# Optimization experiments

Hardware: AMD Instinct MI355X
Metric: run time of the kernel (lower is better)

## Reference

```python
import jax, jax.numpy as jnp
import numpy as np

N_NODES = 50000
N_EDGES = 400000
N_GRAPHS = 128
IN_DIM = 768
HID = 128
N_CLASSES = 11
BN_EPS = 1e-5


def _sage_conv(x, src, dst, Wl, bl, Wr):
    # PyG SAGEConv (aggr='mean'): out = lin_l(mean_{j->i} x_j) + lin_r(x_i)
    # messages flow src -> dst; nodes with no in-edges get a zero aggregate.
    n = x.shape[0]
    deg = jax.ops.segment_sum(jnp.ones_like(dst, x.dtype), dst, num_segments=n)
    agg = jax.ops.segment_sum(x[src], dst, num_segments=n)  # [N, d] gather+scatter
    agg = agg / jnp.maximum(deg, 1.0)[:, None]
    return agg @ Wl.T + bl + x @ Wr.T


def _batch_norm(x, gamma, beta):
    # training-mode BatchNorm1d: biased batch statistics over the node axis
    m = jnp.mean(x, axis=0)
    v = jnp.var(x, axis=0)
    return (x - m) * jax.lax.rsqrt(v + BN_EPS) * gamma + beta


def setup_inputs() -> dict:
    key = jax.random.key(0)
    ks = jax.random.split(key, 16)
    x = jax.random.normal(ks[0], (N_NODES, IN_DIM), dtype=jnp.float32)
    edge_index = jax.random.randint(ks[1], (2, N_EDGES), 0, N_NODES, dtype=jnp.int32)
    batch = jnp.sort(jax.random.randint(ks[2], (N_NODES,), 0, N_GRAPHS, dtype=jnp.int32))

    def lin_w(k, out_d, in_d):
        return jax.random.normal(k, (out_d, in_d), dtype=jnp.float32) * (1.0 / np.sqrt(in_d))

    params = {
        'W1l': lin_w(ks[3], HID, IN_DIM), 'b1': jnp.zeros((HID,), jnp.float32),
        'W1r': lin_w(ks[4], HID, IN_DIM),
        'g1': jnp.ones((HID,), jnp.float32), 'be1': jnp.zeros((HID,), jnp.float32),
        'W2l': lin_w(ks[5], HID, HID), 'b2': jnp.zeros((HID,), jnp.float32),
        'W2r': lin_w(ks[6], HID, HID),
        'g2': jnp.ones((HID,), jnp.float32), 'be2': jnp.zeros((HID,), jnp.float32),
        'W3l': lin_w(ks[7], HID, HID), 'b3': jnp.zeros((HID,), jnp.float32),
        'W3r': lin_w(ks[8], HID, HID),
        'g3': jnp.ones((HID,), jnp.float32), 'be3': jnp.zeros((HID,), jnp.float32),
        'Wlin': lin_w(ks[9], N_CLASSES, HID), 'blin': jnp.zeros((N_CLASSES,), jnp.float32),
    }
    return {'x': x, 'edge_index': edge_index, 'batch': batch, **params}


def reference(x, edge_index, batch,
              W1l, b1, W1r, g1, be1,
              W2l, b2, W2r, g2, be2,
              W3l, b3, W3r, g3, be3,
              Wlin, blin):
    src, dst = edge_index[0], edge_index[1]
    h = jax.nn.relu(_batch_norm(_sage_conv(x, src, dst, W1l, b1, W1r), g1, be1))
    h = jax.nn.relu(_batch_norm(_sage_conv(h, src, dst, W2l, b2, W2r), g2, be2))
    h = _batch_norm(_sage_conv(h, src, dst, W3l, b3, W3r), g3, be3)
    # global_max_pool over graph ids
    pooled = jax.ops.segment_max(h, batch, num_segments=N_GRAPHS)  # [G, HID]
    # dropout is identity at inference
    return pooled @ Wlin.T + blin  # [G, 11]
```

## Files before the change

kernel.cpp:

```cpp
#include <hip/hip_runtime.h>

#define N_NODESC 50000
#define N_EDGESC 400000
#define N_GRAPHSC 128
#define IN_DIMC 768
#define HIDC 128
#define NCLSC 11
#define BN_EPSC 1e-5f
#define NB_AGG 8
#define NREP 64
#define SCAN_NB ((N_NODESC + 255) / 256)

typedef __bf16 bf16_t;
typedef __bf16 bf16x2 __attribute__((ext_vector_type(2)));
typedef __bf16 bf16x8 __attribute__((ext_vector_type(8)));
typedef float f32x4 __attribute__((ext_vector_type(4)));

typedef __attribute__((address_space(1))) void glb_void;
typedef __attribute__((address_space(3))) void lds_void;

__device__ __forceinline__ void cp16(const void* g, void* l) {
    __builtin_amdgcn_global_load_lds((glb_void*)g, (lds_void*)l, 16, 0, 0);
}

__device__ __forceinline__ f32x4 mfma_16x16x32_bf16(bf16x8 a, bf16x8 b, f32x4 c) {
    return __builtin_amdgcn_mfma_f32_16x16x32_bf16(a, b, c, 0, 0, 0);
}

template<int MODE, int KC>
__global__ __launch_bounds__(256) void gemm_kernel(const void* __restrict__ Av,
                                                   const bf16_t* __restrict__ Wb,
                                                   const float* __restrict__ stats,
                                                   const float* __restrict__ g,
                                                   const float* __restrict__ be,
                                                   bf16_t* __restrict__ Cl,
                                                   bf16_t* __restrict__ Cr,
                                                   int M)
{
    constexpr int NK   = KC / 32;
    constexpr int ASZ  = (MODE == 0) ? 16384 : 8192;
    constexpr int BSZ  = 8192;
    constexpr int NAB  = (MODE == 0) ? 2 : 3;
    constexpr int NBB  = (MODE == 0) ? 2 : 3;
    constexpr int AISS = (MODE == 0) ? 4 : 2;
    constexpr int AKB  = (MODE == 0) ? 128 : 64;
    constexpr int SCSZ = (MODE == 1) ? 1024 : 16;
    __shared__ __align__(16) unsigned char smem[NAB * ASZ + NBB * BSZ + SCSZ];
    unsigned char* Asm = smem;
    unsigned char* Bsm = smem + NAB * ASZ;
    float* scS = (float*)(smem + NAB * ASZ + NBB * BSZ);

    const int t    = threadIdx.x;
    const int m0   = blockIdx.x * 128;
    const int half = blockIdx.y;
    const int wid  = t >> 6;
    const int lane = t & 63;
    const int wm   = (wid >> 1) * 64;
    const int wn   = (wid & 1) * 64;
    const int l16  = lane & 15;
    const int quad = lane >> 4;

    const char* aSrc[AISS]; int aDst[AISS];
#pragma unroll
    for (int s = 0; s < AISS; s++) {
        int L = (s * 4 + wid) * 64 + lane;
        int r, c;
        if (MODE == 0) { r = L >> 3; c = (L & 7) ^ (r & 7); }
        else           { r = L >> 2; c = (L & 3) ^ ((r >> 1) & 3); }
        int row = m0 + r; if (row > M - 1) row = M - 1;
        if (MODE == 0) aSrc[s] = (const char*)Av + ((size_t)row * KC + (size_t)c * 4) * 4;
        else           aSrc[s] = (const char*)Av + ((size_t)row * KC + (size_t)c * 8) * 2;
        aDst[s] = (s * 4 + wid) * 1024;
    }
    const char* bSrc[2]; int bDst[2];
#pragma unroll
    for (int s = 0; s < 2; s++) {
        int L = (s * 4 + wid) * 64 + lane;
        int r = L >> 2;
        int c = (L & 3) ^ ((r >> 1) & 3);
        bSrc[s] = (const char*)(Wb + (size_t)(half * 128 + r) * KC + c * 8);
        bDst[s] = (s * 4 + wid) * 1024;
    }

    int aOff[4][2], bOff[4];
#pragma unroll
    for (int i = 0; i < 4; i++) {
        int ra = wm + i * 16 + l16;
        if (MODE == 0) {
            aOff[i][0] = ra * 128 + (((2 * quad)     ^ (ra & 7)) * 16);
            aOff[i][1] = ra * 128 + (((2 * quad + 1) ^ (ra & 7)) * 16);
        } else {
            aOff[i][0] = ra * 64 + ((quad ^ ((ra >> 1) & 3)) * 16);
            aOff[i][1] = 0;
        }
        int rb = wn + i * 16 + l16;
        bOff[i] = rb * 64 + ((quad ^ ((rb >> 1) & 3)) * 16);
    }

    if (MODE == 1) {
        if (t < HIDC) {
            float sum = 0.f, sumsq = 0.f;
            for (int r = 0; r < NREP; r++) {
                sum   += stats[r * 256 + t];
                sumsq += stats[r * 256 + HIDC + t];
            }
            float invM = 1.0f / (float)M;
            float mean = sum * invM;
            float var  = sumsq * invM - mean * mean;
            float s = rsqrtf(var + BN_EPSC) * g[t];
            scS[t] = s;
            scS[HIDC + t] = be[t] - mean * s;
        }
        __syncthreads();
    }

    f32x4 acc[4][4] = {};

    if constexpr (MODE == 0) {
#pragma unroll
        for (int s = 0; s < 4; s++) cp16(aSrc[s], Asm + aDst[s]);
#pragma unroll
        for (int s = 0; s < 2; s++) cp16(bSrc[s], Bsm + bDst[s]);

        for (int it = 0; it < NK; ++it) {
            if (it + 1 < NK) {
                const size_t ka = (size_t)(it + 1) * 128;
                const size_t kb = (size_t)(it + 1) * 64;
                const int nb = (it + 1) & 1;
#pragma unroll
                for (int s = 0; s < 4; s++) cp16(aSrc[s] + ka, Asm + nb * ASZ + aDst[s]);
#pragma unroll
                for (int s = 0; s < 2; s++) cp16(bSrc[s] + kb, Bsm + nb * BSZ + bDst[s]);
                asm volatile("s_waitcnt vmcnt(6)" ::: "memory");
            } else {
                asm volatile("s_waitcnt vmcnt(0)" ::: "memory");
            }
            asm volatile("s_barrier" ::: "memory");

            const unsigned char* Ab = Asm + (it & 1) * ASZ;
            const unsigned char* Bb = Bsm + (it & 1) * BSZ;
            bf16x8 af[4], bfr[4];
#pragma unroll
            for (int i = 0; i < 4; i++) {
                float4 u0 = *(const float4*)(Ab + aOff[i][0]);
                float4 u1 = *(const float4*)(Ab + aOff[i][1]);
                af[i][0] = (bf16_t)u0.x; af[i][1] = (bf16_t)u0.y;
                af[i][2] = (bf16_t)u0.z; af[i][3] = (bf16_t)u0.w;
                af[i][4] = (bf16_t)u1.x; af[i][5] = (bf16_t)u1.y;
                af[i][6] = (bf16_t)u1.z; af[i][7] = (bf16_t)u1.w;
            }
#pragma unroll
            for (int j = 0; j < 4; j++)
                bfr[j] = *(const bf16x8*)(Bb + bOff[j]);
#pragma unroll
            for (int i = 0; i < 4; i++)
#pragma unroll
                for (int j = 0; j < 4; j++)
                    acc[i][j] = mfma_16x16x32_bf16(af[i], bfr[j], acc[i][j]);

            asm volatile("s_barrier" ::: "memory");
        }
    } else {
#pragma unroll
        for (int s = 0; s < 2; s++) cp16(aSrc[s], Asm + aDst[s]);
#pragma unroll
        for (int s = 0; s < 2; s++) cp16(bSrc[s], Bsm + bDst[s]);
#pragma unroll
        for (int s = 0; s < 2; s++) cp16(aSrc[s] + 64, Asm + ASZ + aDst[s]);
#pragma unroll
        for (int s = 0; s < 2; s++) cp16(bSrc[s] + 64, Bsm + BSZ + bDst[s]);

        for (int it = 0; it < NK; ++it) {
            if (it + 2 < NK) {
                const size_t kb2 = (size_t)(it + 2) * 64;
                const int nb = (it + 2) % 3;
#pragma unroll
                for (int s = 0; s < 2; s++) cp16(aSrc[s] + kb2, Asm + nb * ASZ + aDst[s]);
#pragma unroll
                for (int s = 0; s < 2; s++) cp16(bSrc[s] + kb2, Bsm + nb * BSZ + bDst[s]);
                asm volatile("s_waitcnt vmcnt(8)" ::: "memory");
            } else if (it + 1 < NK) {
                asm volatile("s_waitcnt vmcnt(4)" ::: "memory");
            } else {
                asm volatile("s_waitcnt vmcnt(0)" ::: "memory");
            }
            asm volatile("s_barrier" ::: "memory");

            const unsigned char* Ab = Asm + (it % 3) * ASZ;
            const unsigned char* Bb = Bsm + (it % 3) * BSZ;
            bf16x8 af[4], bfr[4];
            float4 s0 = *(const float4*)&scS[it * 32 + quad * 8];
            float4 s1 = *(const float4*)&scS[it * 32 + quad * 8 + 4];
            float4 h0 = *(const float4*)&scS[HIDC + it * 32 + quad * 8];
            float4 h1 = *(const float4*)&scS[HIDC + it * 32 + quad * 8 + 4];
            float ss[8] = {s0.x, s0.y, s0.z, s0.w, s1.x, s1.y, s1.z, s1.w};
            float hh[8] = {h0.x, h0.y, h0.z, h0.w, h1.x, h1.y, h1.z, h1.w};
#pragma unroll
            for (int i = 0; i < 4; i++) {
                bf16x8 raw = *(const bf16x8*)(Ab + aOff[i][0]);
#pragma unroll
                for (int e = 0; e < 8; e++)
                    af[i][e] = (bf16_t)fmaxf(fmaf((float)raw[e], ss[e], hh[e]), 0.0f);
            }
#pragma unroll
            for (int j = 0; j < 4; j++)
                bfr[j] = *(const bf16x8*)(Bb + bOff[j]);
#pragma unroll
            for (int i = 0; i < 4; i++)
#pragma unroll
                for (int j = 0; j < 4; j++)
                    acc[i][j] = mfma_16x16x32_bf16(af[i], bfr[j], acc[i][j]);

            asm volatile("s_barrier" ::: "memory");
        }
    }

    bf16_t* C = half ? Cr : Cl;
#pragma unroll
    for (int i = 0; i < 4; i++) {
        int rowb = m0 + wm + i * 16 + quad * 4;
#pragma unroll
        for (int j = 0; j < 4; j++) {
            int colh = wn + j * 16 + l16;
#pragma unroll
            for (int rr = 0; rr < 4; rr++) {
                int row = rowb + rr;
                if (row < M) C[(size_t)row * HIDC + colh] = (bf16_t)acc[i][j][rr];
            }
        }
    }
}

__global__ void init_kernel(const float* __restrict__ W1l, const float* __restrict__ W1r,
                            const float* __restrict__ W2l, const float* __restrict__ W2r,
                            const float* __restrict__ W3l, const float* __restrict__ W3r,
                            bf16_t* __restrict__ Wb1, bf16_t* __restrict__ Wb2,
                            bf16_t* __restrict__ Wb3,
                            int* __restrict__ degi, float* __restrict__ stats)
{
    const int NW1 = 128 * IN_DIMC;
    const int NW2 = 128 * HIDC;
    const int NS  = 3 * NREP * 256;
    int j = blockIdx.x * blockDim.x + threadIdx.x;
    if (j < 2 * NW1) { Wb1[j] = (bf16_t)((j < NW1) ? W1l[j] : W1r[j - NW1]); return; }
    j -= 2 * NW1;
    if (j < 2 * NW2) { Wb2[j] = (bf16_t)((j < NW2) ? W2l[j] : W2r[j - NW2]); return; }
    j -= 2 * NW2;
    if (j < 2 * NW2) { Wb3[j] = (bf16_t)((j < NW2) ? W3l[j] : W3r[j - NW2]); return; }
    j -= 2 * NW2;
    if (j < NS) { stats[j] = 0.0f; return; }
    j -= NS;
    if (j < N_NODESC) degi[j] = 0;
}

__global__ void degi_kernel(const int* __restrict__ ei, int* __restrict__ degi) {
    int e = blockIdx.x * blockDim.x + threadIdx.x;
    if (e < N_EDGESC) atomicAdd(&degi[ei[N_EDGESC + e]], 1);
}

__global__ __launch_bounds__(256) void scan1_kernel(const int* __restrict__ degi,
                                                    int* __restrict__ local,
                                                    int* __restrict__ partials)
{
    __shared__ int tmp[256];
    const int t = threadIdx.x;
    const int i = blockIdx.x * 256 + t;
    int v = (i < N_NODESC) ? degi[i] : 0;
    tmp[t] = v;
    __syncthreads();
    for (int off = 1; off < 256; off <<= 1) {
        int u = (t >= off) ? tmp[t - off] : 0;
        __syncthreads();
        tmp[t] += u;
        __syncthreads();
    }
    if (i < N_NODESC) local[i] = tmp[t] - v;
    if (t == 255) partials[blockIdx.x] = tmp[255];
}

__global__ __launch_bounds__(256) void scan3_kernel(const int* __restrict__ local,
                                                    const int* __restrict__ partials,
                                                    int* __restrict__ rowptr,
                                                    int* __restrict__ cursor)
{
    __shared__ int inc[256];
    __shared__ int orig[256];
    const int t = threadIdx.x;
    int v = (t < SCAN_NB) ? partials[t] : 0;
    inc[t] = v; orig[t] = v;
    __syncthreads();
    for (int off = 1; off < 256; off <<= 1) {
        int u = (t >= off) ? inc[t - off] : 0;
        __syncthreads();
        inc[t] += u;
        __syncthreads();
    }
    const int boff = inc[blockIdx.x] - orig[blockIdx.x];
    const int i = blockIdx.x * 256 + t;
    if (i < N_NODESC) {
        int r = local[i] + boff;
        rowptr[i] = r;
        cursor[i] = r;
    }
    if (i == 0) rowptr[N_NODESC] = N_EDGESC;
}

__global__ void fill_kernel(const int* __restrict__ ei, int* __restrict__ cursor,
                            int* __restrict__ col) {
    int e = blockIdx.x * blockDim.x + threadIdx.x;
    if (e >= N_EDGESC) return;
    int d = ei[N_EDGESC + e];
    int pos = atomicAdd(&cursor[d], 1);
    col[pos] = ei[e];
}

__global__ __launch_bounds__(128) void agg_combine_kernel(const int* __restrict__ rowptr,
                                                          const int* __restrict__ col,
                                                          const bf16_t* __restrict__ Plb,
                                                          const bf16_t* __restrict__ Prb,
                                                          const float* __restrict__ bias,
                                                          bf16_t* __restrict__ Hb,
                                                          float* __restrict__ stats, int M)
{
    const int lane = threadIdx.x & 63;
    const int wv   = threadIdx.x >> 6;
    const int c0   = lane * 2;
    const float b0 = bias[c0], b1v = bias[c0 + 1];
    float s0 = 0.f, s1 = 0.f, q0 = 0.f, q1 = 0.f;
    const int n0 = blockIdx.x * NB_AGG + wv * (NB_AGG / 2);
    for (int rr = 0; rr < NB_AGG / 2; rr++) {
        int n = n0 + rr;
        if (n >= M) break;
        int lo = rowptr[n], hi = rowptr[n + 1];
        float a0 = 0.f, a1 = 0.f;
        for (int e = lo; e < hi; e += 8) {
            int rem = hi - e;
            int idx[8];
#pragma unroll
            for (int j = 0; j < 8; j++) {
                int ee = e + j; if (ee > hi - 1) ee = hi - 1;
                idx[j] = col[ee];
            }
            bf16x2 v[8];
#pragma unroll
            for (int j = 0; j < 8; j++)
                v[j] = *(const bf16x2*)&Plb[(size_t)idx[j] * HIDC + c0];
#pragma unroll
            for (int j = 0; j < 8; j++)
                if (j < rem) { a0 += (float)v[j][0]; a1 += (float)v[j][1]; }
        }
        int d = hi - lo;
        float inv = 1.0f / (float)(d > 0 ? d : 1);
        bf16x2 pr = *(const bf16x2*)&Prb[(size_t)n * HIDC + c0];
        float pre0 = fmaf(a0, inv, b0) + (float)pr[0];
        float pre1 = fmaf(a1, inv, b1v) + (float)pr[1];
        bf16x2 hv; hv[0] = (bf16_t)pre0; hv[1] = (bf16_t)pre1;
        *(bf16x2*)&Hb[(size_t)n * HIDC + c0] = hv;
        s0 += pre0; s1 += pre1; q0 += pre0 * pre0; q1 += pre1 * pre1;
    }
    const int rep = (blockIdx.x * 2 + wv) & (NREP - 1);
    atomicAdd(&stats[rep * 256 + c0], s0);
    atomicAdd(&stats[rep * 256 + c0 + 1], s1);
    atomicAdd(&stats[rep * 256 + HIDC + c0], q0);
    atomicAdd(&stats[rep * 256 + HIDC + c0 + 1], q1);
}

__global__ __launch_bounds__(128) void poolhead_kernel(const bf16_t* __restrict__ Hb,
                                                       const float* __restrict__ stats,
                                                       const float* __restrict__ g,
                                                       const float* __restrict__ be,
                                                       const int* __restrict__ batch,
                                                       const float* __restrict__ Wlin,
                                                       const float* __restrict__ blin,
                                                       float* __restrict__ out, int M)
{
    __shared__ float sp[HIDC];
    int gph = blockIdx.x;
    int c   = threadIdx.x;
    float sum = 0.f, sumsq = 0.f;
    for (int r = 0; r < NREP; r++) {
        sum   += stats[r * 256 + c];
        sumsq += stats[r * 256 + HIDC + c];
    }
    float invM = 1.0f / (float)M;
    float mean = sum * invM;
    float var  = sumsq * invM - mean * mean;
    float s = rsqrtf(var + BN_EPSC) * g[c];
    float h = be[c] - mean * s;

    int lo = 0, hi = M;
    while (lo < hi) { int m = (lo + hi) >> 1; if (batch[m] < gph) lo = m + 1; else hi = m; }
    int lo2 = lo, hi2 = M;
    while (lo2 < hi2) { int m = (lo2 + hi2) >> 1; if (batch[m] < gph + 1) lo2 = m + 1; else hi2 = m; }
    float mx = -INFINITY;
    for (int rr = lo; rr < lo2; rr++)
        mx = fmaxf(mx, fmaf((float)Hb[(size_t)rr * HIDC + c], s, h));
    sp[c] = mx;
    __syncthreads();
    if (c < NCLSC) {
        float acc = blin[c];
        for (int k = 0; k < HIDC; k++) acc += sp[k] * Wlin[c * HIDC + k];
        out[gph * NCLSC + c] = acc;
    }
}

extern "C" void kernel_launch(void* const* d_in, const int* in_sizes, int n_in,
                              void* d_out, int out_size, void* d_ws, size_t ws_size,
                              hipStream_t stream)
{
    const float* x     = (const float*)d_in[0];
    const int*   ei    = (const int*)d_in[1];
    const int*   batch = (const int*)d_in[2];
    const float* W1l = (const float*)d_in[3];
    const float* b1  = (const float*)d_in[4];
    const float* W1r = (const float*)d_in[5];
    const float* g1  = (const float*)d_in[6];
    const float* be1 = (const float*)d_in[7];
    const float* W2l = (const float*)d_in[8];
    const float* b2  = (const float*)d_in[9];
    const float* W2r = (const float*)d_in[10];
    const float* g2  = (const float*)d_in[11];
    const float* be2 = (const float*)d_in[12];
    const float* W3l = (const float*)d_in[13];
    const float* b3  = (const float*)d_in[14];
    const float* W3r = (const float*)d_in[15];
    const float* g3  = (const float*)d_in[16];
    const float* be3 = (const float*)d_in[17];
    const float* Wlin = (const float*)d_in[18];
    const float* blin = (const float*)d_in[19];

    const int M = N_NODESC;

    char* w = (char*)d_ws;
    bf16_t* Plb  = (bf16_t*)w;  w += (size_t)M * HIDC * 2;
    bf16_t* Prb  = (bf16_t*)w;  w += (size_t)M * HIDC * 2;
    bf16_t* Hb   = (bf16_t*)w;  w += (size_t)M * HIDC * 2;
    bf16_t* Wb1  = (bf16_t*)w;  w += (size_t)256 * IN_DIMC * 2;
    bf16_t* Wb2  = (bf16_t*)w;  w += (size_t)256 * HIDC * 2;
    bf16_t* Wb3  = (bf16_t*)w;  w += (size_t)256 * HIDC * 2;
    int*   rowptr= (int*)w;     w += (size_t)(M + 16) * 4;
    int*   col   = (int*)w;     w += (size_t)N_EDGESC * 4;
    int*   cursor= (int*)w;     w += (size_t)M * 4;
    int*   degi  = (int*)w;     w += (size_t)M * 4;
    int*   slocal= (int*)w;     w += (size_t)M * 4;
    int*   spart = (int*)w;     w += 256 * 4;
    float* stats = (float*)w;   w += (size_t)3 * NREP * 256 * 4;

    float* stats1 = stats;
    float* stats2 = stats + NREP * 256;
    float* stats3 = stats + 2 * NREP * 256;

    const dim3 gemm_grid((M + 127) / 128, 2);
    const int agg_blocks = (M + NB_AGG - 1) / NB_AGG;
    const int init_total = 2 * 128 * IN_DIMC + 4 * 128 * HIDC + 3 * NREP * 256 + M;

    init_kernel<<<(init_total + 255) / 256, 256, 0, stream>>>(W1l, W1r, W2l, W2r, W3l, W3r,
                                                              Wb1, Wb2, Wb3, degi, stats);
    degi_kernel<<<(N_EDGESC + 255) / 256, 256, 0, stream>>>(ei, degi);
    scan1_kernel<<<SCAN_NB, 256, 0, stream>>>(degi, slocal, spart);
    scan3_kernel<<<SCAN_NB, 256, 0, stream>>>(slocal, spart, rowptr, cursor);
    fill_kernel<<<(N_EDGESC + 255) / 256, 256, 0, stream>>>(ei, cursor, col);

    gemm_kernel<0, IN_DIMC><<<gemm_grid, 256, 0, stream>>>(x, Wb1, nullptr, nullptr, nullptr,
                                                           Plb, Prb, M);
    agg_combine_kernel<<<agg_blocks, 128, 0, stream>>>(rowptr, col, Plb, Prb, b1, Hb, stats1, M);

    gemm_kernel<1, HIDC><<<gemm_grid, 256, 0, stream>>>(Hb, Wb2, stats1, g1, be1, Plb, Prb, M);
    agg_combine_kernel<<<agg_blocks, 128, 0, stream>>>(rowptr, col, Plb, Prb, b2, Hb, stats2, M);

    gemm_kernel<1, HIDC><<<gemm_grid, 256, 0, stream>>>(Hb, Wb3, stats2, g2, be2, Plb, Prb, M);
    agg_combine_kernel<<<agg_blocks, 128, 0, stream>>>(rowptr, col, Plb, Prb, b3, Hb, stats3, M);

    poolhead_kernel<<<N_GRAPHSC, 128, 0, stream>>>(Hb, stats3, g3, be3, batch, Wlin, blin,
                                                   (float*)d_out, M);
}
```

Before: 578.5 us.

## Convert fp32 A tiles to bf16 in registers before LDS, triple-buffer layer-1 GEMM

Measured after the change: 593.4 us. 2.6% more time.

```diff
diff --git a/kernel.cpp b/kernel.cpp
--- a/kernel.cpp
+++ b/kernel.cpp
@@ -38,21 +38,21 @@
                                                    int M)
 {
     constexpr int NK   = KC / 32;
-    constexpr int ASZ  = (MODE == 0) ? 16384 : 8192;
+    constexpr int ASZ  = 8192;
     constexpr int BSZ  = 8192;
-    constexpr int NAB  = (MODE == 0) ? 2 : 3;
-    constexpr int NBB  = (MODE == 0) ? 2 : 3;
-    constexpr int AISS = (MODE == 0) ? 4 : 2;
-    constexpr int AKB  = (MODE == 0) ? 128 : 64;
     constexpr int SCSZ = (MODE == 1) ? 1024 : 16;
-    __shared__ __align__(16) unsigned char smem[NAB * ASZ + NBB * BSZ + SCSZ];
+    __shared__ __align__(16) unsigned char smem[3 * ASZ + 3 * BSZ + SCSZ];
     unsigned char* Asm = smem;
-    unsigned char* Bsm = smem + NAB * ASZ;
-    float* scS = (float*)(smem + NAB * ASZ + NBB * BSZ);
+    unsigned char* Bsm = smem + 3 * ASZ;
+    float* scS = (float*)(smem + 3 * ASZ + 3 * BSZ);
+
+    const int bid  = blockIdx.x;
+    const int p    = ((bid >> 4) << 3) + (bid & 7);
+    const int half = (bid >> 3) & 1;
+    if (p * 128 >= M) return;
+    const int m0 = p * 128;
 
     const int t    = threadIdx.x;
-    const int m0   = blockIdx.x * 128;
-    const int half = blockIdx.y;
     const int wid  = t >> 6;
     const int lane = t & 63;
     const int wm   = (wid >> 1) * 64;
@@ -60,18 +60,6 @@
     const int l16  = lane & 15;
     const int quad = lane >> 4;
 
-    const char* aSrc[AISS]; int aDst[AISS];
-#pragma unroll
-    for (int s = 0; s < AISS; s++) {
-        int L = (s * 4 + wid) * 64 + lane;
-        int r, c;
-        if (MODE == 0) { r = L >> 3; c = (L & 7) ^ (r & 7); }
-        else           { r = L >> 2; c = (L & 3) ^ ((r >> 1) & 3); }
-        int row = m0 + r; if (row > M - 1) row = M - 1;
-        if (MODE == 0) aSrc[s] = (const char*)Av + ((size_t)row * KC + (size_t)c * 4) * 4;
-        else           aSrc[s] = (const char*)Av + ((size_t)row * KC + (size_t)c * 8) * 2;
-        aDst[s] = (s * 4 + wid) * 1024;
-    }
     const char* bSrc[2]; int bDst[2];
 #pragma unroll
     for (int s = 0; s < 2; s++) {
@@ -82,19 +70,34 @@
         bDst[s] = (s * 4 + wid) * 1024;
     }
 
-    int aOff[4][2], bOff[4];
+    const char* aSrc[2]; int aDst[2];
+    if constexpr (MODE == 1) {
+#pragma unroll
+        for (int s = 0; s < 2; s++) {
+            int L = (s * 4 + wid) * 64 + lane;
+            int r = L >> 2;
+            int c = (L & 3) ^ ((r >> 1) & 3);
+            int row = m0 + r; if (row > M - 1) row = M - 1;
+            aSrc[s] = (const char*)Av + ((size_t)row * KC + (size_t)c * 8) * 2;
+            aDst[s] = (s * 4 + wid) * 1024;
+        }
+    }
+
+    const int rL = (wid << 5) + (lane >> 1);
+    int rAg = m0 + rL; if (rAg > M - 1) rAg = M - 1;
+    const int hA = lane & 1;
+    const float* aG = (const float*)Av + (size_t)rAg * KC + hA * 16;
+    const int cA0 = hA * 2;
+    const int wb0 = rL * 64 + (((cA0)     ^ ((rL >> 1) & 3)) << 4);
+    const int wb1 = rL * 64 + (((cA0 + 1) ^ ((rL >> 1) & 3)) << 4);
+
+    int aOff[4], bOff[4];
 #pragma unroll
     for (int i = 0; i < 4; i++) {
         int ra = wm + i * 16 + l16;
-        if (MODE == 0) {
-            aOff[i][0] = ra * 128 + (((2 * quad)     ^ (ra & 7)) * 16);
-            aOff[i][1] = ra * 128 + (((2 * quad + 1) ^ (ra & 7)) * 16);
-        } else {
-            aOff[i][0] = ra * 64 + ((quad ^ ((ra >> 1) & 3)) * 16);
-            aOff[i][1] = 0;
-        }
+        aOff[i] = ra * 64 + ((quad ^ ((ra >> 1) & 3)) << 4);
         int rb = wn + i * 16 + l16;
-        bOff[i] = rb * 64 + ((quad ^ ((rb >> 1) & 3)) * 16);
+        bOff[i] = rb * 64 + ((quad ^ ((rb >> 1) & 3)) << 4);
     }
 
     if (MODE == 1) {
@@ -116,39 +119,54 @@
 
     f32x4 acc[4][4] = {};
 
+#define ALD(IT, G0, G1, G2, G3) { \
+        const float4* _p = (const float4*)(aG + (size_t)(IT) * 32); \
+        G0 = _p[0]; G1 = _p[1]; G2 = _p[2]; G3 = _p[3]; }
+#define CVTW(G0, G1, G2, G3, DST) { \
+        bf16x8 _w0, _w1; \
+        _w0[0]=(bf16_t)G0.x; _w0[1]=(bf16_t)G0.y; _w0[2]=(bf16_t)G0.z; _w0[3]=(bf16_t)G0.w; \
+        _w0[4]=(bf16_t)G1.x; _w0[5]=(bf16_t)G1.y; _w0[6]=(bf16_t)G1.z; _w0[7]=(bf16_t)G1.w; \
+        _w1[0]=(bf16_t)G2.x; _w1[1]=(bf16_t)G2.y; _w1[2]=(bf16_t)G2.z; _w1[3]=(bf16_t)G2.w; \
+        _w1[4]=(bf16_t)G3.x; _w1[5]=(bf16_t)G3.y; _w1[6]=(bf16_t)G3.z; _w1[7]=(bf16_t)G3.w; \
+        *(bf16x8*)((DST) + wb0) = _w0; *(bf16x8*)((DST) + wb1) = _w1; }
+
     if constexpr (MODE == 0) {
-#pragma unroll
-        for (int s = 0; s < 4; s++) cp16(aSrc[s], Asm + aDst[s]);
+        float4 gaA0, gaA1, gaA2, gaA3;
+        float4 gaB0, gaB1, gaB2, gaB3;
+
+        ALD(0, gaA0, gaA1, gaA2, gaA3);
 #pragma unroll
         for (int s = 0; s < 2; s++) cp16(bSrc[s], Bsm + bDst[s]);
+        ALD(1, gaB0, gaB1, gaB2, gaB3);
+#pragma unroll
+        for (int s = 0; s < 2; s++) cp16(bSrc[s] + 64, Bsm + BSZ + bDst[s]);
+        CVTW(gaA0, gaA1, gaA2, gaA3, Asm);
 
         for (int it = 0; it < NK; ++it) {
+            if (it + 1 < NK) asm volatile("s_waitcnt vmcnt(6) lgkmcnt(0)" ::: "memory");
+            else             asm volatile("s_waitcnt vmcnt(0) lgkmcnt(0)" ::: "memory");
+            asm volatile("s_barrier" ::: "memory");
+
+            if (it + 2 < NK) {
+                const size_t kb = (size_t)(it + 2) * 64;
+                const int nb = (it + 2) % 3;
+#pragma unroll
+                for (int s = 0; s < 2; s++) cp16(bSrc[s] + kb, Bsm + nb * BSZ + bDst[s]);
+                if ((it & 1) == 0) { ALD(it + 2, gaA0, gaA1, gaA2, gaA3); }
+                else               { ALD(it + 2, gaB0, gaB1, gaB2, gaB3); }
+            }
             if (it + 1 < NK) {
-                const size_t ka = (size_t)(it + 1) * 128;
-                const size_t kb = (size_t)(it + 1) * 64;
-                const int nb = (it + 1) & 1;
-#pragma unroll
-                for (int s = 0; s < 4; s++) cp16(aSrc[s] + ka, Asm + nb * ASZ + aDst[s]);
-#pragma unroll
-                for (int s = 0; s < 2; s++) cp16(bSrc[s] + kb, Bsm + nb * BSZ + bDst[s]);
-                asm volatile("s_waitcnt vmcnt(6)" ::: "memory");
-            } else {
-                asm volatile("s_waitcnt vmcnt(0)" ::: "memory");
-            }
-            asm volatile("s_barrier" ::: "memory");
-
-            const unsigned char* Ab = Asm + (it & 1) * ASZ;
-            const unsigned char* Bb = Bsm + (it & 1) * BSZ;
+                unsigned char* Ad = Asm + ((it + 1) % 3) * ASZ;
+                if ((it & 1) == 0) { CVTW(gaB0, gaB1, gaB2, gaB3, Ad); }
+                else               { CVTW(gaA0, gaA1, gaA2, gaA3, Ad); }
+            }
+
+            const unsigned char* Ab = Asm + (it % 3) * ASZ;
+            const unsigned char* Bb = Bsm + (it % 3) * BSZ;
             bf16x8 af[4], bfr[4];
 #pragma unroll
-            for (int i = 0; i < 4; i++) {
-                float4 u0 = *(const float4*)(Ab + aOff[i][0]);
-                float4 u1 = *(const float4*)(Ab + aOff[i][1]);
-                af[i][0] = (bf16_t)u0.x; af[i][1] = (bf16_t)u0.y;
-                af[i][2] = (bf16_t)u0.z; af[i][3] = (bf16_t)u0.w;
-                af[i][4] = (bf16_t)u1.x; af[i][5] = (bf16_t)u1.y;
-                af[i][6] = (bf16_t)u1.z; af[i][7] = (bf16_t)u1.w;
-            }
+            for (int i = 0; i < 4; i++)
+                af[i] = *(const bf16x8*)(Ab + aOff[i]);
 #pragma unroll
             for (int j = 0; j < 4; j++)
                 bfr[j] = *(const bf16x8*)(Bb + bOff[j]);
@@ -157,8 +175,6 @@
 #pragma unroll
                 for (int j = 0; j < 4; j++)
                     acc[i][j] = mfma_16x16x32_bf16(af[i], bfr[j], acc[i][j]);
-
-            asm volatile("s_barrier" ::: "memory");
         }
     } else {
 #pragma unroll
@@ -197,7 +213,7 @@
             float hh[8] = {h0.x, h0.y, h0.z, h0.w, h1.x, h1.y, h1.z, h1.w};
 #pragma unroll
             for (int i = 0; i < 4; i++) {
-                bf16x8 raw = *(const bf16x8*)(Ab + aOff[i][0]);
+                bf16x8 raw = *(const bf16x8*)(Ab + aOff[i]);
 #pragma unroll
                 for (int e = 0; e < 8; e++)
                     af[i][e] = (bf16_t)fmaxf(fmaf((float)raw[e], ss[e], hh[e]), 0.0f);
@@ -214,6 +230,8 @@
             asm volatile("s_barrier" ::: "memory");
         }
     }
+#undef ALD
+#undef CVTW
 
     bf16_t* C = half ? Cr : Cl;
 #pragma unroll
@@ -450,7 +468,8 @@
     float* stats2 = stats + NREP * 256;
     float* stats3 = stats + 2 * NREP * 256;
 
-    const dim3 gemm_grid((M + 127) / 128, 2);
+    const int nP = (M + 127) / 128;
+    const dim3 gemm_grid(((nP + 7) / 8) * 16);
     const int agg_blocks = (M + NB_AGG - 1) / NB_AGG;
     const int init_total = 2 * 128 * IN_DIMC + 4 * 128 * HIDC + 3 * NREP * 256 + M;
 
```
